# Kernel optimization log

Hardware: AMD Instinct MI355X
Metric: run time of the kernel (lower is better)

## Reference

```python
import jax, jax.numpy as jnp
import numpy as np

SMOOTH_WEIGHT = 0.2
SMOOTH_THRESHOLD = 0.2
POS_WEIGHT = 2.0  # class_weight=[2.0]


def setup_inputs() -> dict:
    key = jax.random.key(0)
    k1, k2, k3, k4 = jax.random.split(key, 4)
    B, T, R = 2048, 16, 2048
    return {
        "predictions": jax.random.normal(k1, (B, T, 1), dtype=jnp.float32),
        "region_scores": jax.random.normal(k2, (B, T, R, 1), dtype=jnp.float32),
        "targets": jax.random.randint(k3, (B, T), 0, 2, dtype=jnp.int32),
        "valid_mask": jax.random.randint(k4, (B, T), 0, 2, dtype=jnp.int32),
    }


def reference(predictions, region_scores, targets, valid_mask):
    # predictions: [B, T, 1]; region_scores: [B, T, R, 1]
    y = targets.astype(jnp.float32)[..., None]          # [B, T, 1]
    vm = valid_mask.astype(jnp.float32)[..., None]      # [B, T, 1]

    # BCEWithLogits with pos_weight, reduction='none'
    bce = -(POS_WEIGHT * y * jax.nn.log_sigmoid(predictions)
            + (1.0 - y) * jax.nn.log_sigmoid(-predictions))
    class_loss = (bce * vm).sum() / jnp.maximum(vm.sum(), 1e-8)

    # Smoothness penalty on consecutive region scores where both steps valid
    pair_valid = (vm[:, 1:, 0] > 0.5) & (vm[:, :-1, 0] > 0.5)  # [B, T-1]
    diff = region_scores[:, 1:] - region_scores[:, :-1]        # [B, T-1, R, 1]
    pen = jnp.square(jax.nn.relu(jnp.abs(diff) - SMOOTH_THRESHOLD))
    pen = pen.mean(axis=(2, 3))                                # [B, T-1] mean over regions

    count = pair_valid.sum(axis=0)                             # [T-1] valid samples per step
    pv = pair_valid.astype(pen.dtype)
    step_loss = (pen * pv).sum(axis=0) / jnp.maximum(count, 1) # 0 where count==0
    num_steps = (count > 0).sum()
    smooth_loss = jnp.where(num_steps > 0,
                            step_loss.sum() / jnp.maximum(num_steps, 1),
                            0.0)

    total_loss = class_loss + SMOOTH_WEIGHT * smooth_loss
    return total_loss
```

## Files before the change

### kernel.cpp

```cpp
#include <hip/hip_runtime.h>

#define BB 2048
#define TT 16
#define RR 2048
#define NPAIR (TT - 1)

__device__ __forceinline__ float log_sigmoid(float x) {
    return fminf(x, 0.0f) - log1pf(expf(-fabsf(x)));
}

__global__ void class_loss_kernel(const float* __restrict__ pred,
                                  const int* __restrict__ targets,
                                  const int* __restrict__ vm,
                                  float* __restrict__ ws) {
    int tid = blockIdx.x * blockDim.x + threadIdx.x;
    int stride = gridDim.x * blockDim.x;
    float bce_sum = 0.f, vm_sum = 0.f;
    for (int i = tid; i < BB * TT; i += stride) {
        float x = pred[i];
        float y = (float)targets[i];
        float v = (float)vm[i];
        float bce = -(2.0f * y * log_sigmoid(x) + (1.0f - y) * log_sigmoid(-x));
        bce_sum += bce * v;
        vm_sum += v;
    }
    #pragma unroll
    for (int off = 32; off; off >>= 1) {
        bce_sum += __shfl_down(bce_sum, off);
        vm_sum  += __shfl_down(vm_sum, off);
    }
    __shared__ float s_b[8], s_v[8];
    int lane = threadIdx.x & 63, wave = threadIdx.x >> 6;
    if (lane == 0) { s_b[wave] = bce_sum; s_v[wave] = vm_sum; }
    __syncthreads();
    if (threadIdx.x == 0) {
        float b = 0.f, v = 0.f;
        int nw = blockDim.x >> 6;
        for (int w = 0; w < nw; ++w) { b += s_b[w]; v += s_v[w]; }
        atomicAdd(&ws[0], b);
        atomicAdd(&ws[1], v);
    }
}

__global__ __launch_bounds__(512)
void smooth_kernel(const float* __restrict__ rs,
                   const int* __restrict__ vm,
                   float* __restrict__ S,
                   int* __restrict__ counts) {
    const int b = blockIdx.x >> 1;
    const int h = blockIdx.x & 1;
    const int t0 = h * 8;
    const int np = h ? 7 : 8;
    const int ns = h ? 8 : 9;

    __shared__ int s_vm[TT];
    if (threadIdx.x < TT) s_vm[threadIdx.x] = vm[b * TT + threadIdx.x];
    __syncthreads();

    bool pv[8];
    #pragma unroll
    for (int i = 0; i < 8; ++i) {
        int gp = t0 + i;
        pv[i] = (i < np) && (s_vm[gp] != 0) && (s_vm[gp + 1] != 0);
    }

    const float4* base = (const float4*)(rs + (size_t)b * TT * RR);
    const int r4 = threadIdx.x;

    float4 sl[9];
    #pragma unroll
    for (int i = 0; i < 9; ++i) {
        bool need = (i < ns) && (((i > 0) && pv[i - 1]) || pv[i < 8 ? i : 7] && (i < 8));
        if (i == 8) need = (i < ns) && pv[7];
        if (need) sl[i] = base[(t0 + i) * (RR / 4) + r4];
        else      sl[i] = make_float4(0.f, 0.f, 0.f, 0.f);
    }

    float acc[8];
    #pragma unroll
    for (int p = 0; p < 8; ++p) {
        acc[p] = 0.f;
        if (pv[p]) {
            float dx = fmaxf(fabsf(sl[p + 1].x - sl[p].x) - 0.2f, 0.f);
            float dy = fmaxf(fabsf(sl[p + 1].y - sl[p].y) - 0.2f, 0.f);
            float dz = fmaxf(fabsf(sl[p + 1].z - sl[p].z) - 0.2f, 0.f);
            float dw = fmaxf(fabsf(sl[p + 1].w - sl[p].w) - 0.2f, 0.f);
            acc[p] = dx * dx + dy * dy + dz * dz + dw * dw;
        }
    }

    __shared__ float s_acc[8][8];
    int lane = threadIdx.x & 63, wave = threadIdx.x >> 6;
    #pragma unroll
    for (int p = 0; p < 8; ++p) {
        if (pv[p]) {
            float v = acc[p];
            #pragma unroll
            for (int off = 32; off; off >>= 1) v += __shfl_down(v, off);
            if (lane == 0) s_acc[wave][p] = v;
        }
    }
    __syncthreads();
    if (threadIdx.x < 8) {
        int p = threadIdx.x;
        if (pv[p]) {
            float s = 0.f;
            #pragma unroll
            for (int w = 0; w < 8; ++w) s += s_acc[w][p];
            atomicAdd(&S[t0 + p], s);
            atomicAdd(&counts[t0 + p], 1);
        }
    }
}

__global__ void finalize_kernel(const float* __restrict__ ws,
                                const int* __restrict__ counts,
                                float* __restrict__ out) {
    if (threadIdx.x != 0 || blockIdx.x != 0) return;
    float class_loss = ws[0] / fmaxf(ws[1], 1e-8f);
    float step_sum = 0.f;
    int num_steps = 0;
    for (int p = 0; p < NPAIR; ++p) {
        int c = counts[p];
        float pen_sum = ws[2 + p] / (float)RR;
        float step = pen_sum / (float)(c > 0 ? c : 1);
        step_sum += step;
        if (c > 0) ++num_steps;
    }
    float smooth = (num_steps > 0) ? (step_sum / (float)num_steps) : 0.f;
    out[0] = class_loss + 0.2f * smooth;
}

extern "C" void kernel_launch(void* const* d_in, const int* in_sizes, int n_in,
                              void* d_out, int out_size, void* d_ws, size_t ws_size,
                              hipStream_t stream) {
    const float* pred    = (const float*)d_in[0];
    const float* rs      = (const float*)d_in[1];
    const int*   targets = (const int*)d_in[2];
    const int*   vmask   = (const int*)d_in[3];
    float* out = (float*)d_out;
    float* ws  = (float*)d_ws;
    hipMemsetAsync(d_ws, 0, 32 * sizeof(float), stream);

    class_loss_kernel<<<64, 256, 0, stream>>>(pred, targets, vmask, ws);
    smooth_kernel<<<BB * 2, 512, 0, stream>>>(rs, vmask, ws + 2, (int*)(ws + 17));
    finalize_kernel<<<1, 64, 0, stream>>>(ws, (int*)(ws + 17), out);
}
```

Baseline: 351.5 us.

## Replace global atomics and memset with per-block partials and parallel final reduction

```diff
diff --git a/kernel.cpp b/kernel.cpp
--- a/kernel.cpp
+++ b/kernel.cpp
@@ -4,6 +4,8 @@
 #define TT 16
 #define RR 2048
 #define NPAIR (TT - 1)
+#define NCLS 64
+
 
 __device__ __forceinline__ float log_sigmoid(float x) {
     return fminf(x, 0.0f) - log1pf(expf(-fabsf(x)));
@@ -29,7 +31,7 @@
         bce_sum += __shfl_down(bce_sum, off);
         vm_sum  += __shfl_down(vm_sum, off);
     }
-    __shared__ float s_b[8], s_v[8];
+    __shared__ float s_b[4], s_v[4];
     int lane = threadIdx.x & 63, wave = threadIdx.x >> 6;
     if (lane == 0) { s_b[wave] = bce_sum; s_v[wave] = vm_sum; }
     __syncthreads();
@@ -37,21 +39,19 @@
         float b = 0.f, v = 0.f;
         int nw = blockDim.x >> 6;
         for (int w = 0; w < nw; ++w) { b += s_b[w]; v += s_v[w]; }
-        atomicAdd(&ws[0], b);
-        atomicAdd(&ws[1], v);
+        ws[blockIdx.x] = b;
+        ws[NCLS + blockIdx.x] = v;
     }
 }
 
 __global__ __launch_bounds__(512)
 void smooth_kernel(const float* __restrict__ rs,
                    const int* __restrict__ vm,
-                   float* __restrict__ S,
-                   int* __restrict__ counts) {
+                   float* __restrict__ part) {
     const int b = blockIdx.x >> 1;
     const int h = blockIdx.x & 1;
     const int t0 = h * 8;
     const int np = h ? 7 : 8;
-    const int ns = h ? 8 : 9;
 
     __shared__ int s_vm[TT];
     if (threadIdx.x < TT) s_vm[threadIdx.x] = vm[b * TT + threadIdx.x];
@@ -70,8 +70,7 @@
     float4 sl[9];
     #pragma unroll
     for (int i = 0; i < 9; ++i) {
-        bool need = (i < ns) && (((i > 0) && pv[i - 1]) || pv[i < 8 ? i : 7] && (i < 8));
-        if (i == 8) need = (i < ns) && pv[7];
+        bool need = (i == 0) ? pv[0] : (i == 8) ? pv[7] : (pv[i - 1] || pv[i]);
         if (need) sl[i] = base[(t0 + i) * (RR / 4) + r4];
         else      sl[i] = make_float4(0.f, 0.f, 0.f, 0.f);
     }
@@ -103,32 +102,67 @@
     __syncthreads();
     if (threadIdx.x < 8) {
         int p = threadIdx.x;
+        float s = 0.f;
         if (pv[p]) {
-            float s = 0.f;
             #pragma unroll
             for (int w = 0; w < 8; ++w) s += s_acc[w][p];
-            atomicAdd(&S[t0 + p], s);
-            atomicAdd(&counts[t0 + p], 1);
         }
+        part[(size_t)blockIdx.x * 8 + p] = s;
     }
 }
 
-__global__ void finalize_kernel(const float* __restrict__ ws,
-                                const int* __restrict__ counts,
-                                float* __restrict__ out) {
-    if (threadIdx.x != 0 || blockIdx.x != 0) return;
-    float class_loss = ws[0] / fmaxf(ws[1], 1e-8f);
-    float step_sum = 0.f;
-    int num_steps = 0;
-    for (int p = 0; p < NPAIR; ++p) {
-        int c = counts[p];
-        float pen_sum = ws[2 + p] / (float)RR;
-        float step = pen_sum / (float)(c > 0 ? c : 1);
-        step_sum += step;
-        if (c > 0) ++num_steps;
+__global__ __launch_bounds__(1024)
+void final_kernel(const float* __restrict__ ws,
+                  const int* __restrict__ vm,
+                  float* __restrict__ out) {
+    const float* part = ws + 2 * NCLS;
+    int lane = threadIdx.x & 63, wave = threadIdx.x >> 6;
+
+    __shared__ float s_S[NPAIR];
+    __shared__ int   s_cnt[NPAIR];
+    __shared__ float s_cls[2];
+
+    if (wave < NPAIR) {
+        int p = wave;
+        int h = (p < 8) ? 0 : 1;
+        int i = p - h * 8;
+        float s = 0.f;
+        int cnt = 0;
+        for (int b = lane; b < BB; b += 64) {
+            s += part[(size_t)(2 * b + h) * 8 + i];
+            cnt += (vm[b * TT + p] != 0 && vm[b * TT + p + 1] != 0) ? 1 : 0;
+        }
+        #pragma unroll
+        for (int off = 32; off; off >>= 1) {
+            s += __shfl_down(s, off);
+            cnt += __shfl_down(cnt, off);
+        }
+        if (lane == 0) { s_S[p] = s; s_cnt[p] = cnt; }
+    } else if (wave == 15) {
+        float b = (lane < NCLS) ? ws[lane] : 0.f;
+        float v = (lane < NCLS) ? ws[NCLS + lane] : 0.f;
+        #pragma unroll
+        for (int off = 32; off; off >>= 1) {
+            b += __shfl_down(b, off);
+            v += __shfl_down(v, off);
+        }
+        if (lane == 0) { s_cls[0] = b; s_cls[1] = v; }
     }
-    float smooth = (num_steps > 0) ? (step_sum / (float)num_steps) : 0.f;
-    out[0] = class_loss + 0.2f * smooth;
+    __syncthreads();
+
+    if (threadIdx.x == 0) {
+        float class_loss = s_cls[0] / fmaxf(s_cls[1], 1e-8f);
+        float step_sum = 0.f;
+        int num_steps = 0;
+        for (int p = 0; p < NPAIR; ++p) {
+            int c = s_cnt[p];
+            float pen_sum = s_S[p] / (float)RR;
+            step_sum += pen_sum / (float)(c > 0 ? c : 1);
+            if (c > 0) ++num_steps;
+        }
+        float smooth = (num_steps > 0) ? (step_sum / (float)num_steps) : 0.f;
+        out[0] = class_loss + 0.2f * smooth;
+    }
 }
 
 extern "C" void kernel_launch(void* const* d_in, const int* in_sizes, int n_in,
@@ -140,9 +174,8 @@
     const int*   vmask   = (const int*)d_in[3];
     float* out = (float*)d_out;
     float* ws  = (float*)d_ws;
-    hipMemsetAsync(d_ws, 0, 32 * sizeof(float), stream);
 
-    class_loss_kernel<<<64, 256, 0, stream>>>(pred, targets, vmask, ws);
-    smooth_kernel<<<BB * 2, 512, 0, stream>>>(rs, vmask, ws + 2, (int*)(ws + 17));
-    finalize_kernel<<<1, 64, 0, stream>>>(ws, (int*)(ws + 17), out);
+    class_loss_kernel<<<NCLS, 256, 0, stream>>>(pred, targets, vmask, ws);
+    smooth_kernel<<<BB * 2, 512, 0, stream>>>(rs, vmask, ws + 2 * NCLS);
+    final_kernel<<<1, 1024, 0, stream>>>(ws, vmask, out);
 }
```

New measurement: 367.5 us. 4.6% more time.
